# Performance work log

Measured on AMD Instinct MI355X. Metric: run time of the kernel, lower is better.

Reference implementation:

```python
import jax, jax.numpy as jnp
import numpy as np

EPS = 1e-6  # torch.nn.PairwiseDistance default eps, added to the difference before norm
B, D, H, W = 2048, 1024, 128, 128


def setup_inputs() -> dict:
    key = jax.random.key(0)
    k1, k2 = jax.random.split(key)
    x = jax.random.normal(k1, (B, D), dtype=jnp.float32)
    # SOM codebook: [input_size, H*W], matches torch.randn(input_size, out_size[0]*out_size[1])
    weight = jax.random.normal(k2, (D, H * W), dtype=jnp.float32)
    # grid locations, row-major (x, y) as produced by get_map_index()
    gx, gy = jnp.meshgrid(jnp.arange(H), jnp.arange(W), indexing='ij')
    locations = jnp.stack([gx.ravel(), gy.ravel()], axis=1).astype(jnp.float32)  # [H*W, 2]
    return {"x": x, "weight": weight, "locations": locations}


def reference(x, weight, locations):
    # dists[b, m] = || x[b] - weight[:, m] + EPS ||_2  (PairwiseDistance p=2 semantics)
    d = x.shape[1]
    sq = (jnp.sum(x * x, axis=1, keepdims=True)          # [B, 1]
          + jnp.sum(weight * weight, axis=0)[None, :]    # [1, M]
          - 2.0 * (x @ weight)                            # [B, M] GEMM
          + 2.0 * EPS * (jnp.sum(x, axis=1, keepdims=True) - jnp.sum(weight, axis=0)[None, :])
          + d * EPS * EPS)
    dists = jnp.sqrt(jnp.maximum(sq, 0.0))                # [B, M]
    losses = jnp.min(dists, axis=1, keepdims=True)        # [B, 1]
    bmu_indexes = jnp.argmin(dists, axis=1, keepdims=True)  # [B, 1] int
    bmu_locations = locations[bmu_indexes]                 # [B, 1, 2]
    loss = jnp.sum(losses) / x.shape[0]                    # scalar mean min-distance
    return bmu_indexes, bmu_locations, loss
```

## Files before the change

### kernel.cpp

```cpp
#include <hip/hip_runtime.h>
#include <cstdint>
#include <cstddef>


#define B_  2048
#define D_  1024
#define M_  16384
#define EPS_ 1e-6f

typedef _Float16 v8h __attribute__((ext_vector_type(8)));
typedef float    v4f __attribute__((ext_vector_type(4)));

static __device__ __forceinline__ unsigned long long umin64(unsigned long long a,
                                                            unsigned long long b) {
    return a < b ? a : b;
}

static __device__ __forceinline__ size_t addr16(int r, int c) {
    return (size_t)(r >> 4) * 32768 + (size_t)(c >> 2) * 1024 +
           (size_t)(c & 3) * 256 + (size_t)(r & 15) * 16;
}

#define GLDS16(g, l)                                                            \
    __builtin_amdgcn_global_load_lds(                                           \
        (const __attribute__((address_space(1))) void*)(g),                     \
        (__attribute__((address_space(3))) void*)(l), 16, 0, 0)

__global__ __launch_bounds__(256) void prep(
    const float* __restrict__ x, const float* __restrict__ W,
    _Float16* __restrict__ xh, _Float16* __restrict__ xl,
    _Float16* __restrict__ wth, _Float16* __restrict__ wtl,
    float* __restrict__ rowTerm, float* __restrict__ colTerm,
    unsigned long long* __restrict__ keys, float* __restrict__ out)
{
    const int t = threadIdx.x;
    const int blk = blockIdx.x;
    if (blk < 256) {
        __shared__ float tile[64][65];
        __shared__ float colsq[64];
        if (t < 64) colsq[t] = 0.f;
        const int m0 = blk * 64;
        const int dloc = t >> 4, mq = (t & 15) * 4;
        const int m_local = t & 63, cp = t >> 6;
        for (int dt = 0; dt < 16; ++dt) {
            const int d0 = dt * 64;
            __syncthreads();
            #pragma unroll
            for (int s = 0; s < 4; ++s) {
                float4 v = *(const float4*)(W + (size_t)(d0 + dloc + 16 * s) * M_ + m0 + mq);
                tile[dloc + 16 * s][mq + 0] = v.x;
                tile[dloc + 16 * s][mq + 1] = v.y;
                tile[dloc + 16 * s][mq + 2] = v.z;
                tile[dloc + 16 * s][mq + 3] = v.w;
            }
            __syncthreads();
            v8h h0, l0, h1, l1;
            float part = 0.f;
            #pragma unroll
            for (int e = 0; e < 8; ++e) {
                float v = tile[16 * cp + e][m_local];
                _Float16 hi = (_Float16)v;
                h0[e] = hi; l0[e] = (_Float16)(v - (float)hi);
                part += v * v - 2.0f * EPS_ * v;
            }
            #pragma unroll
            for (int e = 0; e < 8; ++e) {
                float v = tile[16 * cp + 8 + e][m_local];
                _Float16 hi = (_Float16)v;
                h1[e] = hi; l1[e] = (_Float16)(v - (float)hi);
                part += v * v - 2.0f * EPS_ * v;
            }
            atomicAdd(&colsq[m_local], part);
            const int m  = m0 + m_local;
            const int c0 = dt * 8 + 2 * cp;
            const size_t a0 = addr16(m, c0), a1 = addr16(m, c0 + 1);
            *(v8h*)((char*)wth + a0) = h0; *(v8h*)((char*)wth + a1) = h1;
            *(v8h*)((char*)wtl + a0) = l0; *(v8h*)((char*)wtl + a1) = l1;
        }
        __syncthreads();
        if (t < 64) colTerm[m0 + t] = colsq[t];
    } else if (blk < 320) {
        __shared__ float rsum[2];
        const int rb0 = (blk - 256) * 32;
        for (int p = 0; p < 16; ++p) {
            if (t < 2) rsum[t] = 0.f;
            __syncthreads();
            const int r = rb0 + 2 * p + (t >> 7);
            const int c = t & 127;
            float4 q1 = *(const float4*)(x + (size_t)r * D_ + 8 * c);
            float4 q2 = *(const float4*)(x + (size_t)r * D_ + 8 * c + 4);
            float vv[8] = {q1.x, q1.y, q1.z, q1.w, q2.x, q2.y, q2.z, q2.w};
            v8h h, l;
            float part = 0.f;
            #pragma unroll
            for (int e = 0; e < 8; ++e) {
                _Float16 hi = (_Float16)vv[e];
                h[e] = hi; l[e] = (_Float16)(vv[e] - (float)hi);
                part += vv[e] * vv[e] + 2.0f * EPS_ * vv[e];
            }
            const size_t a = addr16(r, c);
            *(v8h*)((char*)xh + a) = h;
            *(v8h*)((char*)xl + a) = l;
            for (int off = 32; off; off >>= 1) part += __shfl_down(part, off, 64);
            if ((t & 63) == 0) atomicAdd(&rsum[t >> 7], part);
            __syncthreads();
            if ((t & 127) == 0) rowTerm[r] = rsum[t >> 7];
            __syncthreads();
        }
    } else {
        for (int i = t; i < B_; i += 256) keys[i] = ~0ull;
        if (t == 0) out[3 * B_] = 0.f;
    }
}

__global__ __launch_bounds__(256, 2) void som_mfma(
    const _Float16* __restrict__ xh, const _Float16* __restrict__ xl,
    const _Float16* __restrict__ wth, const _Float16* __restrict__ wtl,
    const float* __restrict__ rowTerm, const float* __restrict__ colTerm,
    unsigned long long* __restrict__ keys)
{
    __shared__ __align__(16) char smem[49152];
    _Float16* Ah = (_Float16*)smem;
    _Float16* Al = (_Float16*)(smem + 8192);
    _Float16* Bh = (_Float16*)(smem + 16384);
    _Float16* Bl = (_Float16*)(smem + 32768);

    const int t = threadIdx.x;
    const int g = blockIdx.x;
    const int cb = (g >> 4) * 256;
    const int rb = (g & 15) * 128;
    const int L = t & 63, w = t >> 6;
    const int wro = (w >> 1) * 64;
    const int wco = (w & 1) * 128;
    const int c16 = L & 15, kq = L >> 4;

    const int wgrp = t >> 6;
    const int lane16 = (t & 63) * 16;
    const int ldsw = wgrp * 1024;
    const size_t abase0 = (size_t)((rb >> 4) + wgrp) * 32768 + lane16;
    const size_t abase1 = abase0 + 4ull * 32768;
    const size_t bbase0 = (size_t)((cb >> 4) + wgrp) * 32768 + lane16;
    const size_t bbase1 = bbase0 + 4ull * 32768;
    const size_t bbase2 = bbase0 + 8ull * 32768;
    const size_t bbase3 = bbase0 + 12ull * 32768;

    const char* pxh = (const char*)xh;
    const char* pxl = (const char*)xl;
    const char* pwh = (const char*)wth;
    const char* pwl = (const char*)wtl;

    v4f acc[4][8];
    #pragma unroll
    for (int i = 0; i < 4; ++i)
        #pragma unroll
        for (int j = 0; j < 8; ++j) acc[i][j] = (v4f){0.f, 0.f, 0.f, 0.f};

    const int lofs = kq * 128 + c16 * 8;
    int ia[4], ibx[8];
    #pragma unroll
    for (int i = 0; i < 4; ++i) ia[i] = ((wro >> 4) + i) * 512 + lofs;
    #pragma unroll
    for (int j = 0; j < 8; ++j) ibx[j] = ((wco >> 4) + j) * 512 + lofs;

    for (int S = 0; S < 32; ++S) {
        const size_t ko = (size_t)S * 1024;
        __syncthreads();
        GLDS16(pxh + abase0 + ko, smem + ldsw);
        GLDS16(pxh + abase1 + ko, smem + 4096 + ldsw);
        GLDS16(pxl + abase0 + ko, smem + 8192 + ldsw);
        GLDS16(pxl + abase1 + ko, smem + 12288 + ldsw);
        GLDS16(pwh + bbase0 + ko, smem + 16384 + ldsw);
        GLDS16(pwh + bbase1 + ko, smem + 20480 + ldsw);
        GLDS16(pwh + bbase2 + ko, smem + 24576 + ldsw);
        GLDS16(pwh + bbase3 + ko, smem + 28672 + ldsw);
        GLDS16(pwl + bbase0 + ko, smem + 32768 + ldsw);
        GLDS16(pwl + bbase1 + ko, smem + 36864 + ldsw);
        GLDS16(pwl + bbase2 + ko, smem + 40960 + ldsw);
        GLDS16(pwl + bbase3 + ko, smem + 45056 + ldsw);
        __syncthreads();

        v8h ah[4], al4[4], bh4[4], bl4[4];
        #pragma unroll
        for (int i = 0; i < 4; ++i) {
            ah[i]  = *(const v8h*)(Ah + ia[i]);
            al4[i] = *(const v8h*)(Al + ia[i]);
        }
        #pragma unroll
        for (int j = 0; j < 4; ++j) {
            bh4[j] = *(const v8h*)(Bh + ibx[j]);
            bl4[j] = *(const v8h*)(Bl + ibx[j]);
        }
        #pragma unroll
        for (int i = 0; i < 4; ++i)
            #pragma unroll
            for (int j = 0; j < 4; ++j) {
                acc[i][j] = __builtin_amdgcn_mfma_f32_16x16x32_f16(ah[i],  bh4[j], acc[i][j], 0, 0, 0);
                acc[i][j] = __builtin_amdgcn_mfma_f32_16x16x32_f16(ah[i],  bl4[j], acc[i][j], 0, 0, 0);
                acc[i][j] = __builtin_amdgcn_mfma_f32_16x16x32_f16(al4[i], bh4[j], acc[i][j], 0, 0, 0);
            }
        #pragma unroll
        for (int j = 0; j < 4; ++j) {
            bh4[j] = *(const v8h*)(Bh + ibx[j + 4]);
            bl4[j] = *(const v8h*)(Bl + ibx[j + 4]);
        }
        #pragma unroll
        for (int i = 0; i < 4; ++i)
            #pragma unroll
            for (int j = 0; j < 4; ++j) {
                acc[i][j+4] = __builtin_amdgcn_mfma_f32_16x16x32_f16(ah[i],  bh4[j], acc[i][j+4], 0, 0, 0);
                acc[i][j+4] = __builtin_amdgcn_mfma_f32_16x16x32_f16(ah[i],  bl4[j], acc[i][j+4], 0, 0, 0);
                acc[i][j+4] = __builtin_amdgcn_mfma_f32_16x16x32_f16(al4[i], bh4[j], acc[i][j+4], 0, 0, 0);
            }
    }

    float cT[8];
    #pragma unroll
    for (int j = 0; j < 8; ++j) cT[j] = colTerm[cb + wco + j * 16 + c16];
    const float de2 = (float)D_ * EPS_ * EPS_;
    #pragma unroll
    for (int i = 0; i < 4; ++i) {
        #pragma unroll
        for (int r = 0; r < 4; ++r) {
            int row_g = rb + wro + i * 16 + kq * 4 + r;
            float rt = rowTerm[row_g];
            unsigned long long best = ~0ull;
            #pragma unroll
            for (int j = 0; j < 8; ++j) {
                float sq = rt + cT[j] - 2.0f * acc[i][j][r] + de2;
                sq = fmaxf(sq, 0.0f);
                float dist = sqrtf(sq);
                unsigned long long key =
                    ((unsigned long long)__float_as_uint(dist) << 32) |
                    (unsigned int)(cb + wco + j * 16 + c16);
                best = umin64(best, key);
            }
            #pragma unroll
            for (int m = 1; m <= 8; m <<= 1) {
                unsigned long long o =
                    (unsigned long long)__shfl_xor((long long)best, m, 64);
                best = umin64(best, o);
            }
            if (c16 == 0) atomicMin(&keys[row_g], best);
        }
    }
}

__global__ void row_stats(const float* __restrict__ x, float* __restrict__ rowTerm) {
    int b = blockIdx.x;
    const float* xr = x + (size_t)b * D_;
    int t = threadIdx.x;
    float acc = 0.f;
    for (int i = t; i < D_; i += 256) {
        float v = xr[i];
        acc += v * v + 2.0f * EPS_ * v;
    }
    for (int off = 32; off; off >>= 1) acc += __shfl_down(acc, off, 64);
    __shared__ float s[4];
    if ((t & 63) == 0) s[t >> 6] = acc;
    __syncthreads();
    if (t == 0) rowTerm[b] = s[0] + s[1] + s[2] + s[3];
}

__global__ void col_stats(const float* __restrict__ w, float* __restrict__ colTerm) {
    int m = blockIdx.x * 256 + threadIdx.x;
    int d0 = blockIdx.y * 64;
    const float* p = w + (size_t)d0 * M_ + m;
    float acc = 0.f;
    #pragma unroll 8
    for (int d = 0; d < 64; ++d) {
        float v = p[(size_t)d * M_];
        acc += v * v - 2.0f * EPS_ * v;
    }
    atomicAdd(&colTerm[m], acc);
}

__global__ __launch_bounds__(256, 2) void som_gemm(
    const float* __restrict__ A, const float* __restrict__ Wt,
    const float* __restrict__ rowTerm, const float* __restrict__ colTerm,
    unsigned long long* __restrict__ keys)
{
    __shared__ float As[8][128];
    __shared__ float Bs[8][128];
    const int t  = threadIdx.x;
    const int rb = blockIdx.y * 128;
    const int cb = blockIdx.x * 128;
    const int tx = t & 15;
    const int ty = t >> 4;
    float acc[8][8];
    #pragma unroll
    for (int i = 0; i < 8; ++i)
        #pragma unroll
        for (int j = 0; j < 8; ++j) acc[i][j] = 0.f;
    const int la_row = t >> 1, la_k = (t & 1) * 4;
    const int lb_k = t >> 5, lb_n = (t & 31) * 4;
    const float* Aptr = A + (size_t)(rb + la_row) * D_ + la_k;
    const float* Bptr = Wt + (size_t)lb_k * M_ + cb + lb_n;
    for (int k0 = 0; k0 < D_; k0 += 8) {
        float4 av = *(const float4*)(Aptr + k0);
        float4 bv = *(const float4*)(Bptr + (size_t)k0 * M_);
        __syncthreads();
        As[la_k + 0][la_row] = av.x;
        As[la_k + 1][la_row] = av.y;
        As[la_k + 2][la_row] = av.z;
        As[la_k + 3][la_row] = av.w;
        *(float4*)&Bs[lb_k][lb_n] = bv;
        __syncthreads();
        #pragma unroll
        for (int k = 0; k < 8; ++k) {
            float a[8], b[8];
            #pragma unroll
            for (int i = 0; i < 8; ++i) a[i] = As[k][ty * 8 + i];
            #pragma unroll
            for (int j = 0; j < 8; ++j) b[j] = Bs[k][tx * 8 + j];
            #pragma unroll
            for (int i = 0; i < 8; ++i)
                #pragma unroll
                for (int j = 0; j < 8; ++j) acc[i][j] += a[i] * b[j];
        }
    }
    float rT[8], cT[8];
    #pragma unroll
    for (int i = 0; i < 8; ++i) rT[i] = rowTerm[rb + ty * 8 + i];
    #pragma unroll
    for (int j = 0; j < 8; ++j) cT[j] = colTerm[cb + tx * 8 + j];
    const float de2 = (float)D_ * EPS_ * EPS_;
    #pragma unroll
    for (int i = 0; i < 8; ++i) {
        unsigned long long best = ~0ull;
        #pragma unroll
        for (int j = 0; j < 8; ++j) {
            float sq = rT[i] + cT[j] - 2.0f * acc[i][j] + de2;
            sq = fmaxf(sq, 0.0f);
            float dist = sqrtf(sq);
            unsigned long long key =
                ((unsigned long long)__float_as_uint(dist) << 32) |
                (unsigned int)(cb + tx * 8 + j);
            best = umin64(best, key);
        }
        #pragma unroll
        for (int msk = 1; msk <= 8; msk <<= 1) {
            unsigned long long o = __shfl_xor((long long)best, msk, 64);
            best = umin64(best, (unsigned long long)o);
        }
        if (tx == 0) atomicMin(&keys[rb + ty * 8 + i], best);
    }
}

__global__ void finalize(const unsigned long long* __restrict__ keys,
                         const float* __restrict__ loc,
                         float* __restrict__ out)
{
    int t = threadIdx.x;
    int r = blockIdx.x * 256 + t;
    unsigned long long k = keys[r];
    unsigned int idx = (unsigned int)(k & 0xFFFFFFFFu);
    float dist = __uint_as_float((unsigned int)(k >> 32));
    out[r] = (float)idx;
    out[B_ + 2 * r]     = loc[2 * idx];
    out[B_ + 2 * r + 1] = loc[2 * idx + 1];
    float sum = dist;
    for (int off = 32; off; off >>= 1) sum += __shfl_down(sum, off, 64);
    __shared__ float s[4];
    if ((t & 63) == 0) s[t >> 6] = sum;
    __syncthreads();
    if (t == 0) atomicAdd(&out[3 * B_], (s[0] + s[1] + s[2] + s[3]) / (float)B_);
}

extern "C" void kernel_launch(void* const* d_in, const int* in_sizes, int n_in,
                              void* d_out, int out_size, void* d_ws, size_t ws_size,
                              hipStream_t stream)
{
    const float* x   = (const float*)d_in[0];
    const float* w   = (const float*)d_in[1];
    const float* loc = (const float*)d_in[2];
    float* out = (float*)d_out;

    char* ws = (char*)d_ws;
    unsigned long long* keys = (unsigned long long*)ws;
    float* rowTerm = (float*)(ws + (16 << 10));
    float* colTerm = (float*)(ws + (24 << 10));
    _Float16* xh  = (_Float16*)(ws + (1ull << 20));
    _Float16* xl  = (_Float16*)(ws + (5ull << 20));
    _Float16* wth = (_Float16*)(ws + (9ull << 20));
    _Float16* wtl = (_Float16*)(ws + (41ull << 20));
    const size_t NEED = 73ull << 20;

    if (ws_size >= NEED) {
        prep<<<321, 256, 0, stream>>>(x, w, xh, xl, wth, wtl,
                                      rowTerm, colTerm, keys, out);
        som_mfma<<<1024, 256, 0, stream>>>(
            xh, xl, wth, wtl, rowTerm, colTerm, keys);
    } else {
        hipMemsetAsync(keys, 0xFF, B_ * sizeof(unsigned long long), stream);
        hipMemsetAsync(colTerm, 0, M_ * sizeof(float), stream);
        hipMemsetAsync(out + 3 * B_, 0, sizeof(float), stream);
        row_stats<<<B_, 256, 0, stream>>>(x, rowTerm);
        col_stats<<<dim3(M_ / 256, D_ / 64), 256, 0, stream>>>(w, colTerm);
        som_gemm<<<dim3(M_ / 128, B_ / 128), 256, 0, stream>>>(
            x, w, rowTerm, colTerm, keys);
    }
    finalize<<<8, 256, 0, stream>>>(keys, loc, out);
}
```

Before: 310.9 us.

## Parallelize prep across D tiles and double-buffer smaller GEMM tiles

The prep kernel now launches one block per (64 M, 64 D) tile instead of looping over D, accumulating column norms via global atomics after a memset, and row stats use more blocks. The MFMA kernel shrinks its tile from 128x256 to 128x128 with a 2048-block grid and a grouped tile order, and double-buffers LDS so the next K-stage's global-to-LDS loads overlap the current MFMAs. Together these aim to raise parallelism in prep and hide load latency in the GEMM. In exchange the smaller tile lowers per-tile data reuse, adds global atomics, and needs 64KB of LDS, which may reduce occupancy.

```diff
diff --git a/kernel.cpp b/kernel.cpp
--- a/kernel.cpp
+++ b/kernel.cpp
@@ -35,54 +35,50 @@
 {
     const int t = threadIdx.x;
     const int blk = blockIdx.x;
-    if (blk < 256) {
+    if (blk < 4096) {
         __shared__ float tile[64][65];
-        __shared__ float colsq[64];
-        if (t < 64) colsq[t] = 0.f;
-        const int m0 = blk * 64;
+        const int m0 = (blk & 255) * 64;
+        const int d0 = (blk >> 8) * 64;
         const int dloc = t >> 4, mq = (t & 15) * 4;
-        const int m_local = t & 63, cp = t >> 6;
-        for (int dt = 0; dt < 16; ++dt) {
-            const int d0 = dt * 64;
-            __syncthreads();
-            #pragma unroll
-            for (int s = 0; s < 4; ++s) {
-                float4 v = *(const float4*)(W + (size_t)(d0 + dloc + 16 * s) * M_ + m0 + mq);
-                tile[dloc + 16 * s][mq + 0] = v.x;
-                tile[dloc + 16 * s][mq + 1] = v.y;
-                tile[dloc + 16 * s][mq + 2] = v.z;
-                tile[dloc + 16 * s][mq + 3] = v.w;
-            }
-            __syncthreads();
-            v8h h0, l0, h1, l1;
-            float part = 0.f;
-            #pragma unroll
-            for (int e = 0; e < 8; ++e) {
-                float v = tile[16 * cp + e][m_local];
-                _Float16 hi = (_Float16)v;
-                h0[e] = hi; l0[e] = (_Float16)(v - (float)hi);
-                part += v * v - 2.0f * EPS_ * v;
-            }
-            #pragma unroll
-            for (int e = 0; e < 8; ++e) {
-                float v = tile[16 * cp + 8 + e][m_local];
-                _Float16 hi = (_Float16)v;
-                h1[e] = hi; l1[e] = (_Float16)(v - (float)hi);
-                part += v * v - 2.0f * EPS_ * v;
-            }
-            atomicAdd(&colsq[m_local], part);
-            const int m  = m0 + m_local;
-            const int c0 = dt * 8 + 2 * cp;
-            const size_t a0 = addr16(m, c0), a1 = addr16(m, c0 + 1);
-            *(v8h*)((char*)wth + a0) = h0; *(v8h*)((char*)wth + a1) = h1;
-            *(v8h*)((char*)wtl + a0) = l0; *(v8h*)((char*)wtl + a1) = l1;
+        #pragma unroll
+        for (int s = 0; s < 4; ++s) {
+            float4 v = *(const float4*)(W + (size_t)(d0 + dloc + 16 * s) * M_ + m0 + mq);
+            tile[dloc + 16 * s][mq + 0] = v.x;
+            tile[dloc + 16 * s][mq + 1] = v.y;
+            tile[dloc + 16 * s][mq + 2] = v.z;
+            tile[dloc + 16 * s][mq + 3] = v.w;
         }
         __syncthreads();
-        if (t < 64) colTerm[m0 + t] = colsq[t];
-    } else if (blk < 320) {
+        const int mloc = t >> 2, j = t & 3;
+        const int dc = j * 16;
+        v8h h0, l0, h1, l1;
+        float part = 0.f;
+        #pragma unroll
+        for (int e = 0; e < 8; ++e) {
+            float v = tile[dc + e][mloc];
+            _Float16 hi = (_Float16)v;
+            h0[e] = hi; l0[e] = (_Float16)(v - (float)hi);
+            part += v * v - 2.0f * EPS_ * v;
+        }
+        #pragma unroll
+        for (int e = 0; e < 8; ++e) {
+            float v = tile[dc + 8 + e][mloc];
+            _Float16 hi = (_Float16)v;
+            h1[e] = hi; l1[e] = (_Float16)(v - (float)hi);
+            part += v * v - 2.0f * EPS_ * v;
+        }
+        const int m  = m0 + mloc;
+        const int c0 = (d0 >> 3) + j * 2;
+        const size_t a0 = addr16(m, c0), a1 = addr16(m, c0 + 1);
+        *(v8h*)((char*)wth + a0) = h0; *(v8h*)((char*)wth + a1) = h1;
+        *(v8h*)((char*)wtl + a0) = l0; *(v8h*)((char*)wtl + a1) = l1;
+        part += __shfl_xor(part, 1, 64);
+        part += __shfl_xor(part, 2, 64);
+        if (j == 0) atomicAdd(&colTerm[m], part);
+    } else if (blk < 4352) {
         __shared__ float rsum[2];
-        const int rb0 = (blk - 256) * 32;
-        for (int p = 0; p < 16; ++p) {
+        const int rb0 = (blk - 4096) * 8;
+        for (int p = 0; p < 4; ++p) {
             if (t < 2) rsum[t] = 0.f;
             __syncthreads();
             const int r = rb0 + 2 * p + (t >> 7);
@@ -119,103 +115,114 @@
     const float* __restrict__ rowTerm, const float* __restrict__ colTerm,
     unsigned long long* __restrict__ keys)
 {
-    __shared__ __align__(16) char smem[49152];
-    _Float16* Ah = (_Float16*)smem;
-    _Float16* Al = (_Float16*)(smem + 8192);
-    _Float16* Bh = (_Float16*)(smem + 16384);
-    _Float16* Bl = (_Float16*)(smem + 32768);
+    __shared__ __align__(16) char smem[65536];
 
     const int t = threadIdx.x;
     const int g = blockIdx.x;
-    const int cb = (g >> 4) * 256;
-    const int rb = (g & 15) * 128;
+    const int colTile = (g & 7) | ((g >> 7) << 3);
+    const int rowTile = (g >> 3) & 15;
+    const int cb = colTile * 128, rb = rowTile * 128;
+
     const int L = t & 63, w = t >> 6;
-    const int wro = (w >> 1) * 64;
-    const int wco = (w & 1) * 128;
+    const int wro = (w >> 1) * 64, wco = (w & 1) * 64;
     const int c16 = L & 15, kq = L >> 4;
 
-    const int wgrp = t >> 6;
-    const int lane16 = (t & 63) * 16;
-    const int ldsw = wgrp * 1024;
-    const size_t abase0 = (size_t)((rb >> 4) + wgrp) * 32768 + lane16;
-    const size_t abase1 = abase0 + 4ull * 32768;
-    const size_t bbase0 = (size_t)((cb >> 4) + wgrp) * 32768 + lane16;
-    const size_t bbase1 = bbase0 + 4ull * 32768;
-    const size_t bbase2 = bbase0 + 8ull * 32768;
-    const size_t bbase3 = bbase0 + 12ull * 32768;
+    const size_t sa0 = (size_t)((rb >> 4) + (t >> 6)) * 32768 + (t & 63) * 16;
+    const size_t sa1 = sa0 + 4ull * 32768;
+    const size_t sb0 = (size_t)((cb >> 4) + (t >> 6)) * 32768 + (t & 63) * 16;
+    const size_t sb1 = sb0 + 4ull * 32768;
+    const int ldsw = (t & 192) * 16;
 
     const char* pxh = (const char*)xh;
     const char* pxl = (const char*)xl;
     const char* pwh = (const char*)wth;
     const char* pwl = (const char*)wtl;
 
-    v4f acc[4][8];
+    v4f acc[4][4];
     #pragma unroll
     for (int i = 0; i < 4; ++i)
         #pragma unroll
-        for (int j = 0; j < 8; ++j) acc[i][j] = (v4f){0.f, 0.f, 0.f, 0.f};
+        for (int j = 0; j < 4; ++j) acc[i][j] = (v4f){0.f, 0.f, 0.f, 0.f};
 
     const int lofs = kq * 128 + c16 * 8;
-    int ia[4], ibx[8];
+    int ia[4], ib[4];
     #pragma unroll
     for (int i = 0; i < 4; ++i) ia[i] = ((wro >> 4) + i) * 512 + lofs;
     #pragma unroll
-    for (int j = 0; j < 8; ++j) ibx[j] = ((wco >> 4) + j) * 512 + lofs;
-
-    for (int S = 0; S < 32; ++S) {
-        const size_t ko = (size_t)S * 1024;
+    for (int j = 0; j < 4; ++j) ib[j] = ((wco >> 4) + j) * 512 + lofs;
+
+    #define STAGE(off, S)                                                       \
+        do {                                                                    \
+            const size_t ko = (size_t)(S) * 1024;                               \
+            GLDS16(pxh + sa0 + ko, smem + (off) + ldsw);                        \
+            GLDS16(pxh + sa1 + ko, smem + (off) + 4096 + ldsw);                 \
+            GLDS16(pxl + sa0 + ko, smem + (off) + 8192 + ldsw);                 \
+            GLDS16(pxl + sa1 + ko, smem + (off) + 12288 + ldsw);                \
+            GLDS16(pwh + sb0 + ko, smem + (off) + 16384 + ldsw);                \
+            GLDS16(pwh + sb1 + ko, smem + (off) + 20480 + ldsw);                \
+            GLDS16(pwl + sb0 + ko, smem + (off) + 24576 + ldsw);                \
+            GLDS16(pwl + sb1 + ko, smem + (off) + 28672 + ldsw);                \
+        } while (0)
+
+    #define FRAGS(off)                                                          \
+        do {                                                                    \
+            const _Float16* ba = (const _Float16*)(smem + (off));               \
+            _Pragma("unroll")                                                   \
+            for (int i = 0; i < 4; ++i) {                                       \
+                ah[i] = *(const v8h*)(ba + ia[i]);                              \
+                al[i] = *(const v8h*)(ba + 4096 + ia[i]);                       \
+            }                                                                   \
+            _Pragma("unroll")                                                   \
+            for (int j = 0; j < 4; ++j) {                                       \
+                bh[j] = *(const v8h*)(ba + 8192 + ib[j]);                       \
+                bl[j] = *(const v8h*)(ba + 12288 + ib[j]);                      \
+            }                                                                   \
+        } while (0)
+
+    #define MFMAS                                                               \
+        do {                                                                    \
+            _Pragma("unroll")                                                   \
+            for (int i = 0; i < 4; ++i)                                         \
+                _Pragma("unroll")                                               \
+                for (int j = 0; j < 4; ++j)                                     \
+                    acc[i][j] = __builtin_amdgcn_mfma_f32_16x16x32_f16(         \
+                        ah[i], bh[j], acc[i][j], 0, 0, 0);                      \
+            _Pragma("unroll")                                                   \
+            for (int i = 0; i < 4; ++i)                                         \
+                _Pragma("unroll")                                               \
+                for (int j = 0; j < 4; ++j)                                     \
+                    acc[i][j] = __builtin_amdgcn_mfma_f32_16x16x32_f16(         \
+                        ah[i], bl[j], acc[i][j], 0, 0, 0);                      \
+            _Pragma("unroll")                                                   \
+            for (int i = 0; i < 4; ++i)                                         \
+                _Pragma("unroll")                                               \
+                for (int j = 0; j < 4; ++j)                                     \
+                    acc[i][j] = __builtin_amdgcn_mfma_f32_16x16x32_f16(         \
+                        al[i], bh[j], acc[i][j], 0, 0, 0);                      \
+        } while (0)
+
+    v8h ah[4], al[4], bh[4], bl[4];
+
+    STAGE(0, 0);
+
+    for (int p = 0; p < 16; ++p) {
         __syncthreads();
-        GLDS16(pxh + abase0 + ko, smem + ldsw);
-        GLDS16(pxh + abase1 + ko, smem + 4096 + ldsw);
-        GLDS16(pxl + abase0 + ko, smem + 8192 + ldsw);
-        GLDS16(pxl + abase1 + ko, smem + 12288 + ldsw);
-        GLDS16(pwh + bbase0 + ko, smem + 16384 + ldsw);
-        GLDS16(pwh + bbase1 + ko, smem + 20480 + ldsw);
-        GLDS16(pwh + bbase2 + ko, smem + 24576 + ldsw);
-        GLDS16(pwh + bbase3 + ko, smem + 28672 + ldsw);
-        GLDS16(pwl + bbase0 + ko, smem + 32768 + ldsw);
-        GLDS16(pwl + bbase1 + ko, smem + 36864 + ldsw);
-        GLDS16(pwl + bbase2 + ko, smem + 40960 + ldsw);
-        GLDS16(pwl + bbase3 + ko, smem + 45056 + ldsw);
+        FRAGS(0);
+        STAGE(32768, 2 * p + 1);
+        MFMAS;
         __syncthreads();
-
-        v8h ah[4], al4[4], bh4[4], bl4[4];
-        #pragma unroll
-        for (int i = 0; i < 4; ++i) {
-            ah[i]  = *(const v8h*)(Ah + ia[i]);
-            al4[i] = *(const v8h*)(Al + ia[i]);
-        }
-        #pragma unroll
-        for (int j = 0; j < 4; ++j) {
-            bh4[j] = *(const v8h*)(Bh + ibx[j]);
-            bl4[j] = *(const v8h*)(Bl + ibx[j]);
-        }
-        #pragma unroll
-        for (int i = 0; i < 4; ++i)
-            #pragma unroll
-            for (int j = 0; j < 4; ++j) {
-                acc[i][j] = __builtin_amdgcn_mfma_f32_16x16x32_f16(ah[i],  bh4[j], acc[i][j], 0, 0, 0);
-                acc[i][j] = __builtin_amdgcn_mfma_f32_16x16x32_f16(ah[i],  bl4[j], acc[i][j], 0, 0, 0);
-                acc[i][j] = __builtin_amdgcn_mfma_f32_16x16x32_f16(al4[i], bh4[j], acc[i][j], 0, 0, 0);
-            }
-        #pragma unroll
-        for (int j = 0; j < 4; ++j) {
-            bh4[j] = *(const v8h*)(Bh + ibx[j + 4]);
-            bl4[j] = *(const v8h*)(Bl + ibx[j + 4]);
-        }
-        #pragma unroll
-        for (int i = 0; i < 4; ++i)
-            #pragma unroll
-            for (int j = 0; j < 4; ++j) {
-                acc[i][j+4] = __builtin_amdgcn_mfma_f32_16x16x32_f16(ah[i],  bh4[j], acc[i][j+4], 0, 0, 0);
-                acc[i][j+4] = __builtin_amdgcn_mfma_f32_16x16x32_f16(ah[i],  bl4[j], acc[i][j+4], 0, 0, 0);
-                acc[i][j+4] = __builtin_amdgcn_mfma_f32_16x16x32_f16(al4[i], bh4[j], acc[i][j+4], 0, 0, 0);
-            }
-    }
-
-    float cT[8];
-    #pragma unroll
-    for (int j = 0; j < 8; ++j) cT[j] = colTerm[cb + wco + j * 16 + c16];
+        FRAGS(32768);
+        if (p != 15) STAGE(0, 2 * p + 2);
+        MFMAS;
+    }
+
+    #undef STAGE
+    #undef FRAGS
+    #undef MFMAS
+
+    float cT[4];
+    #pragma unroll
+    for (int j = 0; j < 4; ++j) cT[j] = colTerm[cb + wco + j * 16 + c16];
     const float de2 = (float)D_ * EPS_ * EPS_;
     #pragma unroll
     for (int i = 0; i < 4; ++i) {
@@ -225,7 +232,7 @@
             float rt = rowTerm[row_g];
             unsigned long long best = ~0ull;
             #pragma unroll
-            for (int j = 0; j < 8; ++j) {
+            for (int j = 0; j < 4; ++j) {
                 float sq = rt + cT[j] - 2.0f * acc[i][j][r] + de2;
                 sq = fmaxf(sq, 0.0f);
                 float dist = sqrtf(sq);
@@ -386,9 +393,10 @@
     const size_t NEED = 73ull << 20;
 
     if (ws_size >= NEED) {
-        prep<<<321, 256, 0, stream>>>(x, w, xh, xl, wth, wtl,
-                                      rowTerm, colTerm, keys, out);
-        som_mfma<<<1024, 256, 0, stream>>>(
+        hipMemsetAsync(colTerm, 0, M_ * sizeof(float), stream);
+        prep<<<4353, 256, 0, stream>>>(x, w, xh, xl, wth, wtl,
+                                       rowTerm, colTerm, keys, out);
+        som_mfma<<<2048, 256, 0, stream>>>(
             xh, xl, wth, wtl, rowTerm, colTerm, keys);
     } else {
         hipMemsetAsync(keys, 0xFF, B_ * sizeof(unsigned long long), stream);
```

After: 325.6 us. 1.05x slower.
